# Kernel optimization log

Hardware: AMD Instinct MI355X
Metric: run time of the kernel (lower is better)

Reference implementation:

```python
import jax, jax.numpy as jnp
import numpy as np

B = 4096
D = 1024
N = 100000
KS = (10000, 20000, 50000)


def _l2norm(x):
    # F.normalize(p=2, dim=1, eps=1e-12): x / max(||x||, eps)
    n = jnp.sqrt(jnp.sum(x * x, axis=1, keepdims=True))
    return x / jnp.maximum(n, 1e-12)


def setup_inputs() -> dict:
    key = jax.random.key(0)
    ks = jax.random.split(key, 16)
    inp = {}
    inp["anchor"] = jax.random.normal(ks[0], (B, D), jnp.float32)
    inp["index"] = jax.random.randint(ks[1], (B,), 0, N)
    for i, K in enumerate(KS):
        inp[f"inst2cluster{i}"] = jax.random.randint(ks[2 + i], (N,), 0, K)
        inp[f"centroids{i}"] = jax.random.normal(ks[5 + i], (K, D), jnp.float32)
        # density acts as a per-column temperature; keep it bounded away from 0
        inp[f"density{i}"] = jax.random.uniform(ks[8 + i], (K,), jnp.float32, 0.1, 1.0)
    return inp


def reference(anchor, centroids0, centroids1, centroids2,
              density0, density1, density2,
              index, inst2cluster0, inst2cluster1, inst2cluster2):
    Bn = anchor.shape[0]
    a = _l2norm(anchor)
    rows = jnp.arange(Bn)
    cols = jnp.arange(Bn - 1)
    # negatives[i, j] = sim[i, j + (j >= i)] -> row i without its diagonal entry
    neg_idx = cols[None, :] + (cols[None, :] >= rows[:, None])  # [B, B-1]

    scales = [(inst2cluster0, centroids0, density0),
              (inst2cluster1, centroids1, density1),
              (inst2cluster2, centroids2, density2)]
    n_scales = len(scales)

    loss = jnp.zeros(Bn, anchor.dtype)
    for i2c, cent, dens in scales:
        protos = _l2norm(cent)
        pos_id = i2c[index]                       # [B]
        sim = a @ protos[pos_id].T                # [B, B]
        pos = jnp.diagonal(sim)[:, None]          # [B, 1]
        neg = jnp.take_along_axis(sim, neg_idx, axis=1)  # [B, B-1]
        # torch broadcast: [B, B] / [B] divides column j by temp_proto[j]
        logits = jnp.concatenate([pos, neg], axis=1) / dens[pos_id][None, :]
        # CE with label 0, reduction='none'
        ce = jax.nn.logsumexp(logits, axis=1) - logits[:, 0]
        # faithful to the original: division by len(cluster_result) INSIDE the loop
        loss = (loss + ce) / n_scales
    return loss
```

## Files before the change

kernel.cpp:

```cpp
#include <hip/hip_runtime.h>

#define BB 4096
#define DD 1024
#define RTS (BB + 16)

typedef float f32x4 __attribute__((ext_vector_type(4)));
typedef short bf16x8 __attribute__((ext_vector_type(8)));

__device__ __forceinline__ unsigned short f2bf(float f) {
  unsigned u = __float_as_uint(f);
  unsigned r = u + 0x7fffu + ((u >> 16) & 1u);
  return (unsigned short)(r >> 16);
}

__device__ __forceinline__ void async16(const void* g, void* l) {
  __builtin_amdgcn_global_load_lds(
      (const __attribute__((address_space(1))) void*)g,
      (__attribute__((address_space(3))) void*)l,
      16, 0, 0);
}

__global__ __launch_bounds__(256) void norm_anchor(const float* __restrict__ x,
                                                   unsigned short* __restrict__ y) {
  __shared__ float sred[4];
  const int row = blockIdx.x;
  const int tid = threadIdx.x;
  const float4 v = ((const float4*)(x + (size_t)row * DD))[tid];
  float ss = v.x * v.x + v.y * v.y + v.z * v.z + v.w * v.w;
#pragma unroll
  for (int off = 32; off > 0; off >>= 1) ss += __shfl_xor(ss, off, 64);
  if ((tid & 63) == 0) sred[tid >> 6] = ss;
  __syncthreads();
  const float tot = sred[0] + sred[1] + sred[2] + sred[3];
  const float inv = 1.0f / fmaxf(sqrtf(tot), 1e-12f);
  ushort4 o;
  o.x = f2bf(v.x * inv);
  o.y = f2bf(v.y * inv);
  o.z = f2bf(v.z * inv);
  o.w = f2bf(v.w * inv);
  ((ushort4*)(y + (size_t)row * DD))[tid] = o;
}

__global__ __launch_bounds__(256) void gather_norm(
    const int* __restrict__ index,
    const int* __restrict__ i2c0, const int* __restrict__ i2c1, const int* __restrict__ i2c2,
    const float* __restrict__ c0, const float* __restrict__ c1, const float* __restrict__ c2,
    const float* __restrict__ d0, const float* __restrict__ d1, const float* __restrict__ d2,
    unsigned short* __restrict__ p16, float* __restrict__ rt,
    float* __restrict__ rowacc) {
  __shared__ float sred[4];
  const int j = blockIdx.x;
  const int s = blockIdx.y;
  const int tid = threadIdx.x;
  const int* i2c = (s == 0) ? i2c0 : (s == 1) ? i2c1 : i2c2;
  const float* cent = (s == 0) ? c0 : (s == 1) ? c1 : c2;
  const float* dens = (s == 0) ? d0 : (s == 1) ? d1 : d2;
  const int pid = i2c[index[j]];
  const float4 v = ((const float4*)(cent + (size_t)pid * DD))[tid];
  float ss = v.x * v.x + v.y * v.y + v.z * v.z + v.w * v.w;
#pragma unroll
  for (int off = 32; off > 0; off >>= 1) ss += __shfl_xor(ss, off, 64);
  if ((tid & 63) == 0) sred[tid >> 6] = ss;
  __syncthreads();
  const float tot = sred[0] + sred[1] + sred[2] + sred[3];
  const float inv = 1.0f / fmaxf(sqrtf(tot), 1e-12f);
  unsigned short* out = p16 + ((size_t)s * BB + j) * DD;
  ushort4 o;
  o.x = f2bf(v.x * inv);
  o.y = f2bf(v.y * inv);
  o.z = f2bf(v.z * inv);
  o.w = f2bf(v.w * inv);
  ((ushort4*)out)[tid] = o;
  if (tid == 0) rt[(size_t)s * RTS + j] = 1.0f / dens[pid];
  if (tid == 1) rowacc[(size_t)s * BB + j] = 0.0f;
}

__global__ __launch_bounds__(256) void gemm_ce_fused(const unsigned short* __restrict__ A,
                                                     const unsigned short* __restrict__ P,
                                                     const float* __restrict__ rt,
                                                     float* __restrict__ rowacc,
                                                     float* __restrict__ diag) {
  __shared__ __align__(16) unsigned short lA[128 * 32];
  __shared__ __align__(16) unsigned short lB[128 * 32];
  __shared__ float rowsum[2][128];
  const int tid = threadIdx.x;
  const int lane = tid & 63;
  const int wave = tid >> 6;
  const int m0 = blockIdx.y * 128;
  const int n0 = blockIdx.x * 128;
  const int s = blockIdx.z;
  const unsigned short* Bm = P + (size_t)s * BB * DD;
  const float* rt_s = rt + (size_t)s * RTS;

  f32x4 acc[4][4];
#pragma unroll
  for (int mi = 0; mi < 4; ++mi)
#pragma unroll
    for (int ni = 0; ni < 4; ++ni) acc[mi][ni] = (f32x4){0.f, 0.f, 0.f, 0.f};

  const int srow = lane >> 2;
  const int scol = (lane & 3) * 8;

  const int wm = (wave >> 1) * 64;
  const int wn = (wave & 1) * 64;
  const int fr = lane & 15;
  const int fk = (lane >> 4) * 8;

  for (int k0 = 0; k0 < DD; k0 += 32) {
#pragma unroll
    for (int c = 0; c < 2; ++c) {
      const int chunk = wave * 2 + c;
      const int r = chunk * 16 + srow;
      const unsigned short* ga = A + (size_t)(m0 + r) * DD + k0 + scol;
      const unsigned short* gb = Bm + (size_t)(n0 + r) * DD + k0 + scol;
      async16(ga, &lA[chunk * 512]);
      async16(gb, &lB[chunk * 512]);
    }
    __syncthreads();

    bf16x8 af[4], bfr[4];
#pragma unroll
    for (int mi = 0; mi < 4; ++mi)
      af[mi] = *(const bf16x8*)&lA[(wm + mi * 16 + fr) * 32 + fk];
#pragma unroll
    for (int ni = 0; ni < 4; ++ni)
      bfr[ni] = *(const bf16x8*)&lB[(wn + ni * 16 + fr) * 32 + fk];
#pragma unroll
    for (int mi = 0; mi < 4; ++mi)
#pragma unroll
      for (int ni = 0; ni < 4; ++ni)
        acc[mi][ni] = __builtin_amdgcn_mfma_f32_16x16x32_bf16(af[mi], bfr[ni], acc[mi][ni], 0, 0, 0);
    __syncthreads();
  }

  const int cm = (lane >> 4) * 4;
  const float rt0 = rt_s[0];
  float rtc[4], rtp[4];
#pragma unroll
  for (int ni = 0; ni < 4; ++ni) {
    const int col = n0 + wn + ni * 16 + fr;
    rtc[ni] = rt_s[col];
    rtp[ni] = rt_s[col + 1];
  }
#pragma unroll
  for (int mi = 0; mi < 4; ++mi) {
#pragma unroll
    for (int r = 0; r < 4; ++r) {
      const int rowi = m0 + wm + mi * 16 + cm + r;
      float esum = 0.f;
#pragma unroll
      for (int ni = 0; ni < 4; ++ni) {
        const int col = n0 + wn + ni * 16 + fr;
        const float v = acc[mi][ni][r];
        const float rr = (col == rowi) ? rt0 : ((col < rowi) ? rtp[ni] : rtc[ni]);
        const float l = v * rr;
        if (col == rowi) diag[(size_t)s * BB + rowi] = l;
        esum += __expf(l);
      }
#pragma unroll
      for (int off = 1; off < 16; off <<= 1) esum += __shfl_xor(esum, off, 64);
      if (fr == 0) rowsum[wave & 1][wm + mi * 16 + cm + r] = esum;
    }
  }
  __syncthreads();
  for (int t = tid; t < 128; t += 256)
    atomicAdd(&rowacc[(size_t)s * BB + m0 + t], rowsum[0][t] + rowsum[1][t]);
}

__global__ __launch_bounds__(256) void finish(const float* __restrict__ rowacc,
                                              const float* __restrict__ diag,
                                              float* __restrict__ out) {
  const int i = blockIdx.x * 256 + threadIdx.x;
  const float ce0 = logf(rowacc[i]) - diag[i];
  const float ce1 = logf(rowacc[BB + i]) - diag[BB + i];
  const float ce2 = logf(rowacc[2 * BB + i]) - diag[2 * BB + i];
  out[i] = ce0 * (1.0f / 27.0f) + ce1 * (1.0f / 9.0f) + ce2 * (1.0f / 3.0f);
}

extern "C" void kernel_launch(void* const* d_in, const int* in_sizes, int n_in,
                              void* d_out, int out_size, void* d_ws, size_t ws_size,
                              hipStream_t stream) {
  const float* anchor = (const float*)d_in[0];
  const int* index    = (const int*)d_in[1];
  const int* i2c0     = (const int*)d_in[2];
  const float* c0     = (const float*)d_in[3];
  const float* de0    = (const float*)d_in[4];
  const int* i2c1     = (const int*)d_in[5];
  const float* c1     = (const float*)d_in[6];
  const float* de1    = (const float*)d_in[7];
  const int* i2c2     = (const int*)d_in[8];
  const float* c2     = (const float*)d_in[9];
  const float* de2    = (const float*)d_in[10];

  char* ws = (char*)d_ws;
  const size_t A16_OFF = 0;
  const size_t P16_OFF = A16_OFF + (size_t)BB * DD * 2;
  const size_t RT_OFF  = P16_OFF + (size_t)3 * BB * DD * 2;
  const size_t ACC_OFF = RT_OFF + (size_t)3 * RTS * 4;
  const size_t DIA_OFF = ACC_OFF + (size_t)3 * BB * 4;

  unsigned short* a16 = (unsigned short*)(ws + A16_OFF);
  unsigned short* p16 = (unsigned short*)(ws + P16_OFF);
  float* rt     = (float*)(ws + RT_OFF);
  float* rowacc = (float*)(ws + ACC_OFF);
  float* diag   = (float*)(ws + DIA_OFF);
  float* out = (float*)d_out;

  norm_anchor<<<BB, 256, 0, stream>>>(anchor, a16);
  gather_norm<<<dim3(BB, 3), 256, 0, stream>>>(index, i2c0, i2c1, i2c2,
                                               c0, c1, c2, de0, de1, de2, p16, rt, rowacc);
  gemm_ce_fused<<<dim3(BB / 128, BB / 128, 3), 256, 0, stream>>>(a16, p16, rt, rowacc, diag);
  finish<<<BB / 256, 256, 0, stream>>>(rowacc, diag, out);
}
```

Baseline: 442.0 us.

## Enlarge GEMM tiles to 256x256 with 4-stage async LDS pipeline and swizzle

The fused GEMM+CE kernel now uses 256x256 tiles with 8 waves and 512 threads. A 4-deep ring of LDS buffers is filled by async global-to-LDS loads, paced by explicit vmcnt waits and raw barriers, with loads interleaved between two MFMA half-phases. LDS rows use an XOR swizzle to avoid bank conflicts, and MFMA sections run at raised wave priority. This is meant to hide global load latency and raise data reuse per tile, at the cost of 128 KB of LDS, more registers, and fewer blocks (768) to spread across the CUs.

```diff
diff --git a/kernel.cpp b/kernel.cpp
--- a/kernel.cpp
+++ b/kernel.cpp
@@ -3,6 +3,8 @@
 #define BB 4096
 #define DD 1024
 #define RTS (BB + 16)
+#define BK 32
+#define NT (DD / BK)
 
 typedef float f32x4 __attribute__((ext_vector_type(4)));
 typedef short bf16x8 __attribute__((ext_vector_type(8)));
@@ -75,82 +77,121 @@
   if (tid == 1) rowacc[(size_t)s * BB + j] = 0.0f;
 }
 
-__global__ __launch_bounds__(256) void gemm_ce_fused(const unsigned short* __restrict__ A,
-                                                     const unsigned short* __restrict__ P,
-                                                     const float* __restrict__ rt,
-                                                     float* __restrict__ rowacc,
-                                                     float* __restrict__ diag) {
-  __shared__ __align__(16) unsigned short lA[128 * 32];
-  __shared__ __align__(16) unsigned short lB[128 * 32];
-  __shared__ float rowsum[2][128];
+__global__ __launch_bounds__(512, 2) void gemm_ce_fused(const unsigned short* __restrict__ A,
+                                                        const unsigned short* __restrict__ P,
+                                                        const float* __restrict__ rt,
+                                                        float* __restrict__ rowacc,
+                                                        float* __restrict__ diag) {
+  __shared__ __align__(16) unsigned short smem[4][2][8192];
+  __shared__ float rsum[256][4];
   const int tid = threadIdx.x;
   const int lane = tid & 63;
   const int wave = tid >> 6;
-  const int m0 = blockIdx.y * 128;
-  const int n0 = blockIdx.x * 128;
+  const int wm = wave >> 2;
+  const int wn = wave & 3;
+  const int m0 = blockIdx.y * 256;
+  const int n0 = blockIdx.x * 256;
   const int s = blockIdx.z;
   const unsigned short* Bm = P + (size_t)s * BB * DD;
   const float* rt_s = rt + (size_t)s * RTS;
 
-  f32x4 acc[4][4];
-#pragma unroll
-  for (int mi = 0; mi < 4; ++mi)
+  const int row_l = lane >> 2;
+  const int col_e = (((lane & 3) ^ ((row_l >> 1) & 3)) << 3);
+  const int SA = wave * 2;
+  const unsigned short* pA0 = A + (size_t)(m0 + SA * 16 + row_l) * DD + col_e;
+  const unsigned short* pA1 = pA0 + (size_t)16 * DD;
+  const unsigned short* pB0 = Bm + (size_t)(n0 + SA * 16 + row_l) * DD + col_e;
+  const unsigned short* pB1 = pB0 + (size_t)16 * DD;
+
+#pragma unroll
+  for (int tt = 0; tt < 3; ++tt) {
+    async16(pA0 + tt * BK, &smem[tt][0][SA * 512]);
+    async16(pA1 + tt * BK, &smem[tt][0][(SA + 1) * 512]);
+    async16(pB0 + tt * BK, &smem[tt][1][SA * 512]);
+    async16(pB1 + tt * BK, &smem[tt][1][(SA + 1) * 512]);
+  }
+  const unsigned short* qA0 = pA0 + 3 * BK;
+  const unsigned short* qA1 = pA1 + 3 * BK;
+  const unsigned short* qB0 = pB0 + 3 * BK;
+  const unsigned short* qB1 = pB1 + 3 * BK;
+
+  const int fr = lane & 15;
+  const int fq = lane >> 4;
+  const int aoff = fr * 32 + ((fq ^ ((fr >> 1) & 3)) << 3);
+
+  f32x4 acc[8][4];
+#pragma unroll
+  for (int mi = 0; mi < 8; ++mi)
 #pragma unroll
     for (int ni = 0; ni < 4; ++ni) acc[mi][ni] = (f32x4){0.f, 0.f, 0.f, 0.f};
 
-  const int srow = lane >> 2;
-  const int scol = (lane & 3) * 8;
-
-  const int wm = (wave >> 1) * 64;
-  const int wn = (wave & 1) * 64;
-  const int fr = lane & 15;
-  const int fk = (lane >> 4) * 8;
-
-  for (int k0 = 0; k0 < DD; k0 += 32) {
-#pragma unroll
-    for (int c = 0; c < 2; ++c) {
-      const int chunk = wave * 2 + c;
-      const int r = chunk * 16 + srow;
-      const unsigned short* ga = A + (size_t)(m0 + r) * DD + k0 + scol;
-      const unsigned short* gb = Bm + (size_t)(n0 + r) * DD + k0 + scol;
-      async16(ga, &lA[chunk * 512]);
-      async16(gb, &lB[chunk * 512]);
+  for (int t = 0; t < NT; ++t) {
+    const int bt = t & 3;
+    const int bs = (t + 3) & 3;
+    const bool stg = (t + 3 < NT);
+    if (t < NT - 2)        asm volatile("s_waitcnt vmcnt(8)" ::: "memory");
+    else if (t == NT - 2)  asm volatile("s_waitcnt vmcnt(4)" ::: "memory");
+    else                   asm volatile("s_waitcnt vmcnt(0)" ::: "memory");
+    __builtin_amdgcn_s_barrier();
+    asm volatile("" ::: "memory");
+
+    const unsigned short* la = &smem[bt][0][0];
+    const unsigned short* lb = &smem[bt][1][0];
+
+    if (stg) {
+      async16(qA0, &smem[bs][0][SA * 512]);
+      async16(qB0, &smem[bs][1][SA * 512]);
     }
-    __syncthreads();
-
-    bf16x8 af[4], bfr[4];
+    bf16x8 af[4], bv[4];
+#pragma unroll
+    for (int i = 0; i < 4; ++i) af[i] = *(const bf16x8*)&la[(wm * 8 + i) * 512 + aoff];
+#pragma unroll
+    for (int i = 0; i < 4; ++i) bv[i] = *(const bf16x8*)&lb[(wn * 4 + i) * 512 + aoff];
+    __builtin_amdgcn_s_barrier();
+    __builtin_amdgcn_s_setprio(1);
 #pragma unroll
     for (int mi = 0; mi < 4; ++mi)
-      af[mi] = *(const bf16x8*)&lA[(wm + mi * 16 + fr) * 32 + fk];
-#pragma unroll
-    for (int ni = 0; ni < 4; ++ni)
-      bfr[ni] = *(const bf16x8*)&lB[(wn + ni * 16 + fr) * 32 + fk];
+#pragma unroll
+      for (int ni = 0; ni < 4; ++ni)
+        acc[mi][ni] = __builtin_amdgcn_mfma_f32_16x16x32_bf16(af[mi], bv[ni], acc[mi][ni], 0, 0, 0);
+    __builtin_amdgcn_s_setprio(0);
+    __builtin_amdgcn_s_barrier();
+
+    if (stg) {
+      async16(qA1, &smem[bs][0][(SA + 1) * 512]);
+      async16(qB1, &smem[bs][1][(SA + 1) * 512]);
+      qA0 += BK; qA1 += BK; qB0 += BK; qB1 += BK;
+    }
+#pragma unroll
+    for (int i = 0; i < 4; ++i) af[i] = *(const bf16x8*)&la[(wm * 8 + 4 + i) * 512 + aoff];
+    __builtin_amdgcn_s_barrier();
+    __builtin_amdgcn_s_setprio(1);
 #pragma unroll
     for (int mi = 0; mi < 4; ++mi)
 #pragma unroll
       for (int ni = 0; ni < 4; ++ni)
-        acc[mi][ni] = __builtin_amdgcn_mfma_f32_16x16x32_bf16(af[mi], bfr[ni], acc[mi][ni], 0, 0, 0);
-    __syncthreads();
-  }
-
-  const int cm = (lane >> 4) * 4;
+        acc[4 + mi][ni] = __builtin_amdgcn_mfma_f32_16x16x32_bf16(af[mi], bv[ni], acc[4 + mi][ni], 0, 0, 0);
+    __builtin_amdgcn_s_setprio(0);
+  }
+
+  const int cm = fq * 4;
   const float rt0 = rt_s[0];
   float rtc[4], rtp[4];
 #pragma unroll
   for (int ni = 0; ni < 4; ++ni) {
-    const int col = n0 + wn + ni * 16 + fr;
+    const int col = n0 + wn * 64 + ni * 16 + fr;
     rtc[ni] = rt_s[col];
     rtp[ni] = rt_s[col + 1];
   }
 #pragma unroll
-  for (int mi = 0; mi < 4; ++mi) {
+  for (int mi = 0; mi < 8; ++mi) {
 #pragma unroll
     for (int r = 0; r < 4; ++r) {
-      const int rowi = m0 + wm + mi * 16 + cm + r;
+      const int rowi = m0 + wm * 128 + mi * 16 + cm + r;
       float esum = 0.f;
 #pragma unroll
       for (int ni = 0; ni < 4; ++ni) {
-        const int col = n0 + wn + ni * 16 + fr;
+        const int col = n0 + wn * 64 + ni * 16 + fr;
         const float v = acc[mi][ni][r];
         const float rr = (col == rowi) ? rt0 : ((col < rowi) ? rtp[ni] : rtc[ni]);
         const float l = v * rr;
@@ -159,12 +200,14 @@
       }
 #pragma unroll
       for (int off = 1; off < 16; off <<= 1) esum += __shfl_xor(esum, off, 64);
-      if (fr == 0) rowsum[wave & 1][wm + mi * 16 + cm + r] = esum;
+      if (fr == 0) rsum[wm * 128 + mi * 16 + cm + r][wn] = esum;
     }
   }
   __syncthreads();
-  for (int t = tid; t < 128; t += 256)
-    atomicAdd(&rowacc[(size_t)s * BB + m0 + t], rowsum[0][t] + rowsum[1][t]);
+  if (tid < 256) {
+    const float v = rsum[tid][0] + rsum[tid][1] + rsum[tid][2] + rsum[tid][3];
+    atomicAdd(&rowacc[(size_t)s * BB + m0 + tid], v);
+  }
 }
 
 __global__ __launch_bounds__(256) void finish(const float* __restrict__ rowacc,
@@ -209,6 +252,6 @@
   norm_anchor<<<BB, 256, 0, stream>>>(anchor, a16);
   gather_norm<<<dim3(BB, 3), 256, 0, stream>>>(index, i2c0, i2c1, i2c2,
                                                c0, c1, c2, de0, de1, de2, p16, rt, rowacc);
-  gemm_ce_fused<<<dim3(BB / 128, BB / 128, 3), 256, 0, stream>>>(a16, p16, rt, rowacc, diag);
+  gemm_ce_fused<<<dim3(BB / 256, BB / 256, 3), 512, 0, stream>>>(a16, p16, rt, rowacc, diag);
   finish<<<BB / 256, 256, 0, stream>>>(rowacc, diag, out);
 }
```

Measured after the change: 472.1 us. 6.8% more time.
